# Kernel tuning notes

Hardware: AMD Instinct MI355X
Metric: run time of the kernel (lower is better)

Reference implementation:

```python
import jax, jax.numpy as jnp
import numpy as np

D_K = 64
N_HEADS = 16
D_MODEL = 1024
EPS = 1e-5


def setup_inputs() -> dict:
    key = jax.random.key(0)
    ks = jax.random.split(key, 8)
    B, S = 2, 2048
    scale = 1.0 / np.sqrt(D_MODEL)
    inp = {
        "input_Q": jax.random.normal(ks[0], (B, S, D_MODEL), jnp.float32),
        "input_K": jax.random.normal(ks[1], (B, S, D_MODEL), jnp.float32),
        "input_V": jax.random.normal(ks[2], (B, S, D_MODEL), jnp.float32),
        "attn_mask": jax.random.randint(ks[3], (B, S, S), 0, 2) == 1,
        "W_Q": jax.random.normal(ks[4], (D_MODEL, N_HEADS * D_K), jnp.float32) * scale,
        "W_K": jax.random.normal(ks[5], (D_MODEL, N_HEADS * D_K), jnp.float32) * scale,
        "W_V": jax.random.normal(ks[6], (D_MODEL, N_HEADS * D_K), jnp.float32) * scale,
        "W_fc": jax.random.normal(ks[7], (N_HEADS * D_K, D_MODEL), jnp.float32) * scale,
    }
    return inp


def _layer_norm(x):
    mu = jnp.mean(x, axis=-1, keepdims=True)
    var = jnp.var(x, axis=-1, keepdims=True)
    return (x - mu) / jnp.sqrt(var + EPS)


def reference(input_Q, input_K, input_V, attn_mask, W_Q, W_K, W_V, W_fc):
    B, S, _ = input_Q.shape
    # projections -> [B, H, S, d_k]
    Q = (input_Q @ W_Q).reshape(B, S, N_HEADS, D_K).transpose(0, 2, 1, 3)
    K = (input_K @ W_K).reshape(B, S, N_HEADS, D_K).transpose(0, 2, 1, 3)
    V = (input_V @ W_V).reshape(B, S, N_HEADS, D_K).transpose(0, 2, 1, 3)
    scores = jnp.einsum("bhqd,bhkd->bhqk", Q, K) / np.sqrt(D_K)
    scores = jnp.where(attn_mask[:, None, :, :], -1e9, scores)
    attn = jax.nn.softmax(scores, axis=-1)
    context = jnp.einsum("bhqk,bhkd->bhqd", attn, V)
    context = context.transpose(0, 2, 1, 3).reshape(B, S, N_HEADS * D_K)
    output = context @ W_fc
    return _layer_norm(output + input_Q), attn
```

## Files before the change

### kernel.cpp

```cpp
#include <hip/hip_runtime.h>

typedef __bf16 bf16x8 __attribute__((ext_vector_type(8)));
typedef unsigned short u16x8 __attribute__((ext_vector_type(8)));
typedef unsigned short u16x4 __attribute__((ext_vector_type(4)));
typedef float f32x4 __attribute__((ext_vector_type(4)));

#define DEV static __device__ __forceinline__

DEV unsigned short f2bf(float f) {
  union { float f; unsigned u; } v; v.f = f;
  unsigned u = v.u + 0x7FFFu + ((v.u >> 16) & 1u);
  return (unsigned short)(u >> 16);
}

DEV unsigned short f2bf_hw(float f) {
  union { __bf16 b; unsigned short u; } v;
  v.b = (__bf16)f;
  return v.u;
}

DEV float bf2f(unsigned short b) {
  union { unsigned u; float f; } v; v.u = ((unsigned)b) << 16;
  return v.f;
}

DEV float fast_exp2(float x) { return __builtin_amdgcn_exp2f(x); }

DEV int swz(int row, int k) { return row * 64 + (k ^ ((row & 7) * 8)); }

DEV int swzV(int row, int k) {
  return row * 64 + (k ^ ((row & 7) * 8) ^ (((row >> 3) & 7) * 8));
}

#define GLOAD16(gp, lp)                                                        \
  __builtin_amdgcn_global_load_lds(                                            \
      (const __attribute__((address_space(1))) void*)(const void*)(gp),        \
      (__attribute__((address_space(3))) void*)(void*)(lp), 16, 0, 0)

__global__ __launch_bounds__(256) void k_detect(const unsigned* m, int* flag) {
  __shared__ int sF, sI;
  if (threadIdx.x == 0) { sF = 1; sI = 1; }
  __syncthreads();
  int lF = 1, lI = 1;
  for (int i = threadIdx.x; i < 4096; i += 256) {
    unsigned d = m[i];
    lF &= (d == 0u || d == 0x3F800000u);
    lI &= (d == 0u || d == 1u);
  }
  if (!lF) atomicAnd(&sF, 0);
  if (!lI) atomicAnd(&sI, 0);
  __syncthreads();
  if (threadIdx.x == 0) flag[0] = sF ? 2 : (sI ? 0 : 1);
}

__global__ __launch_bounds__(256) void k_pack(const void* m, const int* flag,
                                              unsigned long long* bits) {
  const int tid = threadIdx.x;
  const int w = blockIdx.x * 4 + (tid >> 6);
  const int lane = tid & 63;
  const size_t idx = (size_t)w * 64 + lane;
  const int fl = flag[0];
  int v;
  if (fl == 1)      v = ((const unsigned char*)m)[idx];
  else if (fl == 0) v = ((const int*)m)[idx];
  else              v = (((const float*)m)[idx] != 0.f);
  unsigned long long bal = __ballot(v != 0);
  if (lane == 0) bits[w] = bal;
}

__global__ __launch_bounds__(256) void k_cvt(const float* a, const float* b,
                                             const float* c, unsigned short* out) {
  const int gid = blockIdx.x * 256 + threadIdx.x;
  const int which = gid >> 20;
  const int loc = gid & 1048575;
  const float* src = which == 0 ? a : which == 1 ? b : c;
  float4 f = ((const float4*)src)[loc];
  ushort4 u = make_ushort4(f2bf(f.x), f2bf(f.y), f2bf(f.z), f2bf(f.w));
  *(ushort4*)(out + (size_t)which * 4194304 + (size_t)loc * 4) = u;
}

__global__ __launch_bounds__(256) void k_wt(const float* w0, const float* w1,
                                            const float* w2, const float* w3,
                                            unsigned short* out) {
  __shared__ float t[32][33];
  const int z = blockIdx.z;
  const float* W = z == 0 ? w0 : z == 1 ? w1 : z == 2 ? w2 : w3;
  unsigned short* Wt = out + (size_t)z * 1048576;
  const int x = threadIdx.x, y = threadIdx.y;
  const int k0 = blockIdx.x * 32, n0 = blockIdx.y * 32;
#pragma unroll
  for (int r = 0; r < 4; ++r)
    t[y + r * 8][x] = W[(size_t)(k0 + y + r * 8) * 1024 + n0 + x];
  __syncthreads();
#pragma unroll
  for (int r = 0; r < 4; ++r)
    Wt[(size_t)(n0 + y + r * 8) * 1024 + k0 + x] = f2bf(t[x][y + r * 8]);
}

__global__ __launch_bounds__(256) void k_gemm(
    const unsigned short* __restrict__ A0, const unsigned short* __restrict__ A1,
    const unsigned short* __restrict__ A2, const unsigned short* __restrict__ B0,
    const unsigned short* __restrict__ B1, const unsigned short* __restrict__ B2,
    unsigned short* __restrict__ C0, unsigned short* __restrict__ C1,
    unsigned short* __restrict__ C2, float* __restrict__ Cf) {
  __shared__ __align__(16) unsigned short As[128 * 64];
  __shared__ __align__(16) unsigned short Bs[128 * 64];
  const int z = blockIdx.z;
  const unsigned short* A = z == 0 ? A0 : z == 1 ? A1 : A2;
  const unsigned short* Bt = z == 0 ? B0 : z == 1 ? B1 : B2;
  unsigned short* Cb = z == 0 ? C0 : z == 1 ? C1 : C2;

  const int tid = threadIdx.x, lane = tid & 63, wid = tid >> 6;
  const int mt = blockIdx.x, nt = blockIdx.y;
  const int wm = (wid >> 1) * 64, wn = (wid & 1) * 64;
  const int lr = lane >> 3;
  const int lc = ((lane & 7) ^ (lane >> 3)) * 8;
  const int l15 = lane & 15, lg = lane >> 4;
  f32x4 acc[4][4] = {};

  for (int kt = 0; kt < 16; ++kt) {
    const int k0 = kt * 64;
#pragma unroll
    for (int c = wid; c < 16; c += 4) {
      GLOAD16(A + (size_t)(mt * 128 + c * 8 + lr) * 1024 + k0 + lc, As + c * 512);
      GLOAD16(Bt + (size_t)(nt * 128 + c * 8 + lr) * 1024 + k0 + lc, Bs + c * 512);
    }
    __syncthreads();
#pragma unroll
    for (int ks = 0; ks < 2; ++ks) {
      const int ko = ks * 32 + lg * 8;
      bf16x8 af[4], bfr[4];
#pragma unroll
      for (int f = 0; f < 4; ++f) {
        af[f] = *(const bf16x8*)(As + swz(wm + f * 16 + l15, ko));
        bfr[f] = *(const bf16x8*)(Bs + swz(wn + f * 16 + l15, ko));
      }
#pragma unroll
      for (int i = 0; i < 4; ++i)
#pragma unroll
        for (int j = 0; j < 4; ++j)
          acc[i][j] = __builtin_amdgcn_mfma_f32_16x16x32_bf16(af[i], bfr[j],
                                                              acc[i][j], 0, 0, 0);
    }
    __syncthreads();
  }
  const int rbase = mt * 128 + wm + lg * 4;
  const int cbase = nt * 128 + wn + l15;
#pragma unroll
  for (int i = 0; i < 4; ++i)
#pragma unroll
    for (int j = 0; j < 4; ++j) {
      const int col = cbase + j * 16;
#pragma unroll
      for (int r = 0; r < 4; ++r) {
        const int row = rbase + i * 16 + r;
        if (Cf) Cf[(size_t)row * 1024 + col] = acc[i][j][r];
        else    Cb[(size_t)row * 1024 + col] = f2bf(acc[i][j][r]);
      }
    }
}

__global__ __launch_bounds__(256) void k_attnA(
    const unsigned short* __restrict__ PQ, const unsigned short* __restrict__ PK,
    const unsigned short* __restrict__ PV_, const unsigned long long* __restrict__ bits,
    float* __restrict__ RS, unsigned short* __restrict__ CTX) {
  __shared__ __align__(16) unsigned short KB[2][64 * 64];
  __shared__ __align__(16) unsigned short VB[2][64 * 64];
  __shared__ __align__(16) unsigned short Ps[4][16 * 64];

  const int tid = threadIdx.x, lane = tid & 63, wid = tid >> 6;
  const int qt = blockIdx.x, h = blockIdx.y, b = blockIdx.z;
  const int q0 = qt * 64;
  const int lr = lane >> 3;
  const int lc = ((lane & 7) ^ (lane >> 3)) * 8;
  const int l15 = lane & 15, lg = lane >> 4;
  const size_t rowK = (size_t)(b * 2048) * 1024 + h * 64;
  const float C = 0.125f * 1.44269504f;

#pragma unroll
  for (int c = wid; c < 8; c += 4)
    GLOAD16(PQ + rowK + (size_t)(q0 + c * 8 + lr) * 1024 + lc, KB[0] + c * 512);
  __syncthreads();
  const bf16x8 qf0 = *(const bf16x8*)(KB[0] + swz(wid * 16 + l15, lg * 8));
  const bf16x8 qf1 = *(const bf16x8*)(KB[0] + swz(wid * 16 + l15, 32 + lg * 8));
  const unsigned long long* mrow =
      bits + (size_t)(b * 2048 + q0 + wid * 16 + lg * 4) * 32;
  __syncthreads();

  const int vr = tid >> 3, d0 = (tid & 7) * 8;
  {
#pragma unroll
    for (int c = wid; c < 8; c += 4)
      GLOAD16(PK + rowK + (size_t)(c * 8 + lr) * 1024 + lc, KB[0] + c * 512);
    u16x8 v0 = *(const u16x8*)(PV_ + rowK + (size_t)vr * 1024 + d0);
    u16x8 v1 = *(const u16x8*)(PV_ + rowK + (size_t)(32 + vr) * 1024 + d0);
#pragma unroll
    for (int e = 0; e < 8; ++e) VB[0][swzV(d0 + e, vr)] = v0[e];
#pragma unroll
    for (int e = 0; e < 8; ++e) VB[0][swzV(d0 + e, 32 + vr)] = v1[e];
    __syncthreads();
  }

  float rs[4] = {0.f, 0.f, 0.f, 0.f};
  f32x4 cacc[4] = {};
  int cur = 0;
  for (int kt = 0; kt < 32; ++kt) {
    u16x8 nv0, nv1;
    if (kt < 31) {
      const size_t nb = rowK + (size_t)((kt + 1) * 64) * 1024;
      nv0 = *(const u16x8*)(PV_ + nb + (size_t)vr * 1024 + d0);
      nv1 = *(const u16x8*)(PV_ + nb + (size_t)(32 + vr) * 1024 + d0);
#pragma unroll
      for (int c = wid; c < 8; c += 4)
        GLOAD16(PK + nb + (size_t)(c * 8 + lr) * 1024 + lc, KB[cur ^ 1] + c * 512);
    }
    const unsigned long long wm_[4] = {mrow[kt], mrow[32 + kt], mrow[64 + kt],
                                       mrow[96 + kt]};
#pragma unroll
    for (int fn = 0; fn < 4; ++fn) {
      const bf16x8 kf0 = *(const bf16x8*)(KB[cur] + swz(fn * 16 + l15, lg * 8));
      const bf16x8 kf1 = *(const bf16x8*)(KB[cur] + swz(fn * 16 + l15, 32 + lg * 8));
      f32x4 s = {};
      s = __builtin_amdgcn_mfma_f32_16x16x32_bf16(qf0, kf0, s, 0, 0, 0);
      s = __builtin_amdgcn_mfma_f32_16x16x32_bf16(qf1, kf1, s, 0, 0, 0);
      const int kb = fn * 16 + l15;
#pragma unroll
      for (int r = 0; r < 4; ++r) {
        const float p =
            ((wm_[r] >> kb) & 1) ? 0.f : fast_exp2(s[r] * C);
        rs[r] += p;
        Ps[wid][swz(lg * 4 + r, kb)] = f2bf_hw(p);
      }
    }
#pragma unroll
    for (int ks = 0; ks < 2; ++ks) {
      const int ko = ks * 32 + lg * 8;
      const bf16x8 pf = *(const bf16x8*)(&Ps[wid][swz(l15, ko)]);
#pragma unroll
      for (int fn = 0; fn < 4; ++fn) {
        const bf16x8 vf = *(const bf16x8*)(VB[cur] + swzV(fn * 16 + l15, ko));
        cacc[fn] = __builtin_amdgcn_mfma_f32_16x16x32_bf16(pf, vf, cacc[fn], 0, 0, 0);
      }
    }
    if (kt < 31) {
#pragma unroll
      for (int e = 0; e < 8; ++e) VB[cur ^ 1][swzV(d0 + e, vr)] = nv0[e];
#pragma unroll
      for (int e = 0; e < 8; ++e) VB[cur ^ 1][swzV(d0 + e, 32 + vr)] = nv1[e];
    }
    __syncthreads();
    cur ^= 1;
  }
  float rsr[4];
#pragma unroll
  for (int r = 0; r < 4; ++r) {
#pragma unroll
    for (int m = 1; m < 16; m <<= 1) rs[r] += __shfl_xor(rs[r], m);
    rsr[r] = 1.f / rs[r];
  }
#pragma unroll
  for (int fn = 0; fn < 4; ++fn)
#pragma unroll
    for (int r = 0; r < 4; ++r) {
      const int q = q0 + wid * 16 + lg * 4 + r;
      CTX[(size_t)(b * 2048 + q) * 1024 + h * 64 + fn * 16 + l15] =
          f2bf_hw(cacc[fn][r] * rsr[r]);
    }
  if (l15 == 0) {
#pragma unroll
    for (int r = 0; r < 4; ++r)
      RS[(size_t)(b * 16 + h) * 2048 + q0 + wid * 16 + lg * 4 + r] = rsr[r];
  }
}

__global__ __launch_bounds__(256) void k_attnC(
    const unsigned short* __restrict__ PQ, const unsigned short* __restrict__ PK,
    const unsigned long long* __restrict__ bits, const float* __restrict__ RS,
    float* __restrict__ attn_out) {
  __shared__ __align__(16) unsigned short KB[2][64 * 64];
  __shared__ __align__(16) unsigned short Ps[4][16 * 64];

  const int tid = threadIdx.x, lane = tid & 63, wid = tid >> 6;
  const int qt = blockIdx.x, h = blockIdx.y;
  const int b = blockIdx.z >> 2, kq = blockIdx.z & 3;
  const int ktlo = kq * 8, kthi = ktlo + 8;
  const int q0 = qt * 64;
  const int lr = lane >> 3;
  const int lc = ((lane & 7) ^ (lane >> 3)) * 8;
  const int l15 = lane & 15, lg = lane >> 4;
  const size_t rowK = (size_t)(b * 2048) * 1024 + h * 64;
  const float C = 0.125f * 1.44269504f;

#pragma unroll
  for (int c = wid; c < 8; c += 4)
    GLOAD16(PQ + rowK + (size_t)(q0 + c * 8 + lr) * 1024 + lc, KB[0] + c * 512);
  __syncthreads();
  const bf16x8 qf0 = *(const bf16x8*)(KB[0] + swz(wid * 16 + l15, lg * 8));
  const bf16x8 qf1 = *(const bf16x8*)(KB[0] + swz(wid * 16 + l15, 32 + lg * 8));
  const unsigned long long* mrow =
      bits + (size_t)(b * 2048 + q0 + wid * 16 + lg * 4) * 32;
  float rsr[4];
#pragma unroll
  for (int r = 0; r < 4; ++r)
    rsr[r] = RS[(size_t)(b * 16 + h) * 2048 + q0 + wid * 16 + lg * 4 + r];
  __syncthreads();

#pragma unroll
  for (int c = wid; c < 8; c += 4)
    GLOAD16(PK + rowK + (size_t)(ktlo * 64 + c * 8 + lr) * 1024 + lc,
            KB[0] + c * 512);
  __syncthreads();

  const int srow = lane >> 2, scg = lane & 3;
  float* arow = attn_out + ((size_t)(b * 16 + h) * 2048 + q0 + wid * 16 + srow) * 2048;
  int cur = 0;
  for (int kt = ktlo; kt < kthi; ++kt) {
    const int k0 = kt * 64;
    if (kt < kthi - 1) {
#pragma unroll
      for (int c = wid; c < 8; c += 4)
        GLOAD16(PK + rowK + (size_t)((kt + 1) * 64 + c * 8 + lr) * 1024 + lc,
                KB[cur ^ 1] + c * 512);
    }
    const unsigned long long wm_[4] = {mrow[kt], mrow[32 + kt], mrow[64 + kt],
                                       mrow[96 + kt]};
#pragma unroll
    for (int fn = 0; fn < 4; ++fn) {
      const bf16x8 kf0 = *(const bf16x8*)(KB[cur] + swz(fn * 16 + l15, lg * 8));
      const bf16x8 kf1 = *(const bf16x8*)(KB[cur] + swz(fn * 16 + l15, 32 + lg * 8));
      f32x4 s = {};
      s = __builtin_amdgcn_mfma_f32_16x16x32_bf16(qf0, kf0, s, 0, 0, 0);
      s = __builtin_amdgcn_mfma_f32_16x16x32_bf16(qf1, kf1, s, 0, 0, 0);
      const int kb = fn * 16 + l15;
#pragma unroll
      for (int r = 0; r < 4; ++r) {
        const float p =
            ((wm_[r] >> kb) & 1) ? 0.f : fast_exp2(s[r] * C) * rsr[r];
        Ps[wid][swz(lg * 4 + r, kb)] = f2bf_hw(p);
      }
    }
#pragma unroll
    for (int j = 0; j < 4; ++j) {
      const int c = scg * 4 + j * 16;
      const u16x4 pb = *(const u16x4*)(&Ps[wid][swz(srow, c)]);
      float4 o;
      o.x = bf2f(pb[0]); o.y = bf2f(pb[1]); o.z = bf2f(pb[2]); o.w = bf2f(pb[3]);
      *(float4*)(arow + k0 + c) = o;
    }
    __syncthreads();
    cur ^= 1;
  }
}

__global__ __launch_bounds__(256) void k_ln(const float* __restrict__ PRE,
                                            const float* __restrict__ inQ,
                                            float* __restrict__ out) {
  const int row = blockIdx.x, tid = threadIdx.x;
  const size_t base = (size_t)row * 1024 + tid * 4;
  const float4 x = *(const float4*)(PRE + base);
  const float4 q = *(const float4*)(inQ + base);
  const float v0 = x.x + q.x, v1 = x.y + q.y, v2 = x.z + q.z, v3 = x.w + q.w;
  float s = v0 + v1 + v2 + v3;
  float ss = v0 * v0 + v1 * v1 + v2 * v2 + v3 * v3;
#pragma unroll
  for (int m = 1; m < 64; m <<= 1) {
    s += __shfl_xor(s, m);
    ss += __shfl_xor(ss, m);
  }
  __shared__ float red[8];
  const int wid = tid >> 6, lane = tid & 63;
  if (lane == 0) { red[wid] = s; red[4 + wid] = ss; }
  __syncthreads();
  if (tid == 0) {
    const float S = red[0] + red[1] + red[2] + red[3];
    const float SS = red[4] + red[5] + red[6] + red[7];
    const float mu = S * (1.f / 1024.f);
    const float var = SS * (1.f / 1024.f) - mu * mu;
    red[0] = mu;
    red[1] = rsqrtf(var + 1e-5f);
  }
  __syncthreads();
  const float mu = red[0], rstd = red[1];
  float4 o;
  o.x = (v0 - mu) * rstd; o.y = (v1 - mu) * rstd;
  o.z = (v2 - mu) * rstd; o.w = (v3 - mu) * rstd;
  *(float4*)(out + base) = o;
}

extern "C" void kernel_launch(void* const* d_in, const int* in_sizes, int n_in,
                              void* d_out, int out_size, void* d_ws, size_t ws_size,
                              hipStream_t stream) {
  const float* inQ = (const float*)d_in[0];
  const float* inK = (const float*)d_in[1];
  const float* inV = (const float*)d_in[2];
  const void* msk = d_in[3];
  const float* wq = (const float*)d_in[4];
  const float* wk = (const float*)d_in[5];
  const float* wv = (const float*)d_in[6];
  const float* wf = (const float*)d_in[7];

  char* ws = (char*)d_ws;
  unsigned short* XQ = (unsigned short*)(ws);
  unsigned short* WT = (unsigned short*)(ws + 25165824);
  unsigned short* PQ = (unsigned short*)(ws + 33554432);
  unsigned short* PK = (unsigned short*)(ws + 41943040);
  unsigned short* PV = (unsigned short*)(ws + 50331648);
  unsigned short* CTX = (unsigned short*)(ws + 58720256);
  float* PRE = (float*)(ws + 67108864);
  unsigned long long* BITS = (unsigned long long*)(ws + 83886080);
  float* RS = (float*)(ws + 84934656);
  int* FLAG = (int*)(ws + 85196800);

  float* outLN = (float*)d_out;
  float* outAT = (float*)d_out + 4194304;

  k_detect<<<1, 256, 0, stream>>>((const unsigned*)msk, FLAG);
  k_pack<<<32768, 256, 0, stream>>>(msk, FLAG, BITS);
  k_cvt<<<12288, 256, 0, stream>>>(inQ, inK, inV, XQ);
  k_wt<<<dim3(32, 32, 4), dim3(32, 8, 1), 0, stream>>>(wq, wk, wv, wf, WT);
  k_gemm<<<dim3(32, 8, 3), 256, 0, stream>>>(XQ, XQ + 4194304, XQ + 8388608,
                                             WT, WT + 1048576, WT + 2097152,
                                             PQ, PK, PV, nullptr);
  k_attnA<<<dim3(32, 16, 2), 256, 0, stream>>>(PQ, PK, PV, BITS, RS, CTX);
  k_attnC<<<dim3(32, 16, 8), 256, 0, stream>>>(PQ, PK, BITS, RS, outAT);
  k_gemm<<<dim3(32, 8, 1), 256, 0, stream>>>(CTX, CTX, CTX, WT + 3145728,
                                             WT + 3145728, WT + 3145728,
                                             nullptr, nullptr, nullptr, PRE);
  k_ln<<<4096, 256, 0, stream>>>(PRE, inQ, outLN);
}
```

Before: 364.0 us.

## Split attention KV loop into two halves with a combine kernel

The attention context kernel now splits the 32 key tiles into two halves across a doubled grid, producing unnormalized fp32 partial contexts and row sums. A new combine kernel adds the partials, normalizes, converts to bf16 and writes the reciprocal row sums. The aim is more blocks (2048 instead of 1024) to fill the GPU's compute units and a shorter serial loop per block, at the cost of extra fp32 partial traffic and one more launch. This works without max-rescaling because the softmax uses no max subtraction, so the halves combine by plain addition.

```diff
diff --git a/kernel.cpp b/kernel.cpp
--- a/kernel.cpp
+++ b/kernel.cpp
@@ -160,16 +160,20 @@
     }
 }
 
-__global__ __launch_bounds__(256) void k_attnA(
+__global__ __launch_bounds__(256) void k_attnA2(
     const unsigned short* __restrict__ PQ, const unsigned short* __restrict__ PK,
     const unsigned short* __restrict__ PV_, const unsigned long long* __restrict__ bits,
-    float* __restrict__ RS, unsigned short* __restrict__ CTX) {
+    float* __restrict__ RSP, float* __restrict__ CTXP0, float* __restrict__ CTXP1) {
   __shared__ __align__(16) unsigned short KB[2][64 * 64];
   __shared__ __align__(16) unsigned short VB[2][64 * 64];
   __shared__ __align__(16) unsigned short Ps[4][16 * 64];
 
   const int tid = threadIdx.x, lane = tid & 63, wid = tid >> 6;
-  const int qt = blockIdx.x, h = blockIdx.y, b = blockIdx.z;
+  const int qt = blockIdx.x, h = blockIdx.y;
+  const int b = blockIdx.z & 1, half = blockIdx.z >> 1;
+  const int ktbase = half * 16;
+  float* CP = half ? CTXP1 : CTXP0;
+  float* RP = RSP + half * 65536;
   const int q0 = qt * 64;
   const int lr = lane >> 3;
   const int lc = ((lane & 7) ^ (lane >> 3)) * 8;
@@ -189,11 +193,12 @@
 
   const int vr = tid >> 3, d0 = (tid & 7) * 8;
   {
+    const size_t kb0 = rowK + (size_t)(ktbase * 64) * 1024;
 #pragma unroll
     for (int c = wid; c < 8; c += 4)
-      GLOAD16(PK + rowK + (size_t)(c * 8 + lr) * 1024 + lc, KB[0] + c * 512);
-    u16x8 v0 = *(const u16x8*)(PV_ + rowK + (size_t)vr * 1024 + d0);
-    u16x8 v1 = *(const u16x8*)(PV_ + rowK + (size_t)(32 + vr) * 1024 + d0);
+      GLOAD16(PK + kb0 + (size_t)(c * 8 + lr) * 1024 + lc, KB[0] + c * 512);
+    u16x8 v0 = *(const u16x8*)(PV_ + kb0 + (size_t)vr * 1024 + d0);
+    u16x8 v1 = *(const u16x8*)(PV_ + kb0 + (size_t)(32 + vr) * 1024 + d0);
 #pragma unroll
     for (int e = 0; e < 8; ++e) VB[0][swzV(d0 + e, vr)] = v0[e];
 #pragma unroll
@@ -204,9 +209,9 @@
   float rs[4] = {0.f, 0.f, 0.f, 0.f};
   f32x4 cacc[4] = {};
   int cur = 0;
-  for (int kt = 0; kt < 32; ++kt) {
+  for (int kt = ktbase; kt < ktbase + 16; ++kt) {
     u16x8 nv0, nv1;
-    if (kt < 31) {
+    if (kt < ktbase + 15) {
       const size_t nb = rowK + (size_t)((kt + 1) * 64) * 1024;
       nv0 = *(const u16x8*)(PV_ + nb + (size_t)vr * 1024 + d0);
       nv1 = *(const u16x8*)(PV_ + nb + (size_t)(32 + vr) * 1024 + d0);
@@ -242,7 +247,7 @@
         cacc[fn] = __builtin_amdgcn_mfma_f32_16x16x32_bf16(pf, vf, cacc[fn], 0, 0, 0);
       }
     }
-    if (kt < 31) {
+    if (kt < ktbase + 15) {
 #pragma unroll
       for (int e = 0; e < 8; ++e) VB[cur ^ 1][swzV(d0 + e, vr)] = nv0[e];
 #pragma unroll
@@ -251,26 +256,41 @@
     __syncthreads();
     cur ^= 1;
   }
-  float rsr[4];
 #pragma unroll
   for (int r = 0; r < 4; ++r) {
 #pragma unroll
     for (int m = 1; m < 16; m <<= 1) rs[r] += __shfl_xor(rs[r], m);
-    rsr[r] = 1.f / rs[r];
   }
 #pragma unroll
   for (int fn = 0; fn < 4; ++fn)
 #pragma unroll
     for (int r = 0; r < 4; ++r) {
       const int q = q0 + wid * 16 + lg * 4 + r;
-      CTX[(size_t)(b * 2048 + q) * 1024 + h * 64 + fn * 16 + l15] =
-          f2bf_hw(cacc[fn][r] * rsr[r]);
+      CP[(size_t)(b * 2048 + q) * 1024 + h * 64 + fn * 16 + l15] = cacc[fn][r];
     }
   if (l15 == 0) {
 #pragma unroll
     for (int r = 0; r < 4; ++r)
-      RS[(size_t)(b * 16 + h) * 2048 + q0 + wid * 16 + lg * 4 + r] = rsr[r];
-  }
+      RP[(size_t)(b * 16 + h) * 2048 + q0 + wid * 16 + lg * 4 + r] = rs[r];
+  }
+}
+
+__global__ __launch_bounds__(256) void k_comb(
+    const float* __restrict__ CTXP0, const float* __restrict__ CTXP1,
+    const float* __restrict__ RSP, unsigned short* __restrict__ CTX,
+    float* __restrict__ RS) {
+  const int gid = blockIdx.x * 256 + threadIdx.x;
+  const int row = gid >> 8;
+  const int col = (gid & 255) * 4;
+  const int b = row >> 11, q = row & 2047, h = col >> 6;
+  const size_t ridx = (size_t)(b * 16 + h) * 2048 + q;
+  const float rsr = 1.f / (RSP[ridx] + RSP[65536 + ridx]);
+  const float4 c0 = ((const float4*)CTXP0)[gid];
+  const float4 c1 = ((const float4*)CTXP1)[gid];
+  ushort4 o = make_ushort4(f2bf_hw((c0.x + c1.x) * rsr), f2bf_hw((c0.y + c1.y) * rsr),
+                           f2bf_hw((c0.z + c1.z) * rsr), f2bf_hw((c0.w + c1.w) * rsr));
+  ((ushort4*)CTX)[gid] = o;
+  if ((col & 63) == 0) RS[ridx] = rsr;
 }
 
 __global__ __launch_bounds__(256) void k_attnC(
@@ -407,9 +427,12 @@
   unsigned short* PV = (unsigned short*)(ws + 50331648);
   unsigned short* CTX = (unsigned short*)(ws + 58720256);
   float* PRE = (float*)(ws + 67108864);
+  float* CTXP0 = (float*)(ws + 67108864);
+  float* CTXP1 = (float*)(ws);
   unsigned long long* BITS = (unsigned long long*)(ws + 83886080);
   float* RS = (float*)(ws + 84934656);
-  int* FLAG = (int*)(ws + 85196800);
+  float* RSP = (float*)(ws + 85196800);
+  int* FLAG = (int*)(ws + 85721088);
 
   float* outLN = (float*)d_out;
   float* outAT = (float*)d_out + 4194304;
@@ -421,7 +444,9 @@
   k_gemm<<<dim3(32, 8, 3), 256, 0, stream>>>(XQ, XQ + 4194304, XQ + 8388608,
                                              WT, WT + 1048576, WT + 2097152,
                                              PQ, PK, PV, nullptr);
-  k_attnA<<<dim3(32, 16, 2), 256, 0, stream>>>(PQ, PK, PV, BITS, RS, CTX);
+  k_attnA2<<<dim3(32, 16, 4), 256, 0, stream>>>(PQ, PK, PV, BITS, RSP,
+                                                CTXP0, CTXP1);
+  k_comb<<<4096, 256, 0, stream>>>(CTXP0, CTXP1, RSP, CTX, RS);
   k_attnC<<<dim3(32, 16, 8), 256, 0, stream>>>(PQ, PK, BITS, RS, outAT);
   k_gemm<<<dim3(32, 8, 1), 256, 0, stream>>>(CTX, CTX, CTX, WT + 3145728,
                                              WT + 3145728, WT + 3145728,
```

New measurement: 364.8 us. No clear change (+0.2%).
